# Kernel optimization log

Hardware: AMD Instinct MI355X
Metric: run time of the kernel (lower is better)

Reference implementation:

```python
import jax, jax.numpy as jnp
import numpy as np

EMBED = 1024
HEADS = 16
HEAD_DIM = EMBED // HEADS
SCALE = HEAD_DIM ** -0.5


def setup_inputs() -> dict:
    key = jax.random.key(0)
    ks = jax.random.split(key, 9)
    init = lambda k, shape: jax.random.normal(k, shape, dtype=jnp.float32) * 0.02
    return {
        "hidden_states": jax.random.normal(ks[0], (32, 257, EMBED), dtype=jnp.float32),
        "Wq": init(ks[1], (EMBED, EMBED)), "bq": init(ks[2], (EMBED,)),
        "Wk": init(ks[3], (EMBED, EMBED)), "bk": init(ks[4], (EMBED,)),
        "Wv": init(ks[5], (EMBED, EMBED)), "bv": init(ks[6], (EMBED,)),
        "Wo": init(ks[7], (EMBED, EMBED)), "bo": init(ks[8], (EMBED,)),
    }


def reference(hidden_states, Wq, bq, Wk, bk, Wv, bv, Wo, bo):
    b, t, d = hidden_states.shape
    # projections (torch Linear: x @ W.T + b); scale applied to Q
    q = (hidden_states @ Wq.T + bq) * SCALE
    k = hidden_states @ Wk.T + bk
    v = hidden_states @ Wv.T + bv
    # [b, h, t, hd]
    q = q.reshape(b, t, HEADS, HEAD_DIM).transpose(0, 2, 1, 3)
    k = k.reshape(b, t, HEADS, HEAD_DIM).transpose(0, 2, 1, 3)
    v = v.reshape(b, t, HEADS, HEAD_DIM).transpose(0, 2, 1, 3)
    # attention scores + softmax (dropout p is a no-op in eval mode)
    scores = jnp.einsum("bhqd,bhkd->bhqk", q, k)
    probs = jax.nn.softmax(scores, axis=-1)
    ctx = jnp.einsum("bhqk,bhkd->bhqd", probs, v)
    ctx = ctx.transpose(0, 2, 1, 3).reshape(b, t, d)
    return ctx @ Wo.T + bo
```

## Files before the change

### kernel.cpp

```cpp
#include <hip/hip_runtime.h>


#define B_   32
#define T_   257
#define TP   272
#define H_   16
#define HD_  64
#define D_   1024
#define NTOK 8224
#define BH_  512
#define FRAG_PER_BH 17408

typedef __bf16 bf16;
typedef __bf16 bf16x4 __attribute__((ext_vector_type(4)));
typedef __bf16 bf16x8 __attribute__((ext_vector_type(8)));
typedef short  s16x4  __attribute__((ext_vector_type(4)));
typedef short  s16x8  __attribute__((ext_vector_type(8)));
typedef float  floatx4 __attribute__((ext_vector_type(4)));

static constexpr size_t SZ_XB   = (size_t)NTOK * D_ * 2;
static constexpr size_t SZ_WQKV = (size_t)3 * D_ * D_ * 2;
static constexpr size_t SZ_W    = (size_t)D_ * D_ * 2;
static constexpr size_t SZ_QK   = (size_t)BH_ * FRAG_PER_BH * 2;

static constexpr size_t OFF_XB   = 0;
static constexpr size_t OFF_WQKV = OFF_XB + SZ_XB;
static constexpr size_t OFF_WO   = OFF_WQKV + SZ_WQKV;
static constexpr size_t OFF_Q    = OFF_WO + SZ_W;
static constexpr size_t OFF_K    = OFF_Q + SZ_QK;
static constexpr size_t OFF_V    = OFF_K + SZ_QK;
static constexpr size_t OFF_CTX  = OFF_V + SZ_QK;

#define GLD16(gp, lp)                                                        \
  __builtin_amdgcn_global_load_lds(                                          \
      (const __attribute__((address_space(1))) void*)(gp),                   \
      (__attribute__((address_space(3))) void*)(lp), 16, 0, 0)

__global__ void cast_all_kernel(const float* __restrict__ hs,
                                const float* __restrict__ Wq, const float* __restrict__ Wk,
                                const float* __restrict__ Wv, const float* __restrict__ Wo,
                                bf16* __restrict__ xb, bf16* __restrict__ wqkv,
                                bf16* __restrict__ wob) {
  const int y = blockIdx.y;
  const float* s;
  bf16* d;
  int n4;
  if (y == 0) {
    s = hs; d = xb; n4 = NTOK * D_ / 4;
  } else {
    int z = y - 1;
    s = (z == 0) ? Wq : (z == 1) ? Wk : (z == 2) ? Wv : Wo;
    d = (z < 3) ? wqkv + (size_t)z * D_ * D_ : wob;
    n4 = D_ * D_ / 4;
  }
  int i = blockIdx.x * blockDim.x + threadIdx.x;
  int stride = gridDim.x * blockDim.x;
  for (int idx = i; idx < n4; idx += stride) {
    float4 v = reinterpret_cast<const float4*>(s)[idx];
    bf16x4 o;
    o[0] = (bf16)v.x; o[1] = (bf16)v.y; o[2] = (bf16)v.z; o[3] = (bf16)v.w;
    reinterpret_cast<bf16x4*>(d)[idx] = o;
  }
}



#define KTILE(TT, CC)                                                        \
  do {                                                                       \
    const int ktn_ = ((TT) + 2 < 32) ? (TT) + 2 : 31;                        \
    _Pragma("unroll") for (int mi_ = 0; mi_ < 4; mi_++)                      \
      af[mi_] = *reinterpret_cast<const bf16x8*>(                            \
          smem + (CC) * 8192 + (arow + mi_ * 16) * 32 + qsw);                \
    _Pragma("unroll") for (int nj_ = 0; nj_ < 4; nj_++)                      \
      bfr[nj_] = *reinterpret_cast<const bf16x8*>(                           \
          smem + 16384 + (CC) * 4096 + (brow + nj_ * 16) * 32 + qsw);        \
    asm volatile("s_waitcnt lgkmcnt(0)" ::: "memory");                       \
    __builtin_amdgcn_sched_barrier(0);                                       \
    __builtin_amdgcn_s_barrier();                                            \
                       \
    GLD16(aSrc0 + ktn_ * 32, dstA0 + (CC) * 8192);                           \
    GLD16(aSrc1 + ktn_ * 32, dstA1 + (CC) * 8192);                           \
    GLD16(bSrc + ktn_ * 32, dstB + (CC) * 4096);                             \
    __builtin_amdgcn_sched_barrier(0);                                       \
    __builtin_amdgcn_s_setprio(1);                                           \
    _Pragma("unroll") for (int mi_ = 0; mi_ < 4; mi_++)                      \
      _Pragma("unroll") for (int nj_ = 0; nj_ < 4; nj_++)                    \
        acc[mi_][nj_] = __builtin_amdgcn_mfma_f32_16x16x32_bf16(             \
            af[mi_], bfr[nj_], acc[mi_][nj_], 0, 0, 0);                      \
    __builtin_amdgcn_s_setprio(0);                                           \
    asm volatile("s_waitcnt vmcnt(3)" ::: "memory");                         \
    __builtin_amdgcn_s_barrier();                                            \
  } while (0)

__global__ __launch_bounds__(512, 4) void qkv_gemm(
    const bf16* __restrict__ xb, const bf16* __restrict__ wqkv,
    const float* __restrict__ bq, const float* __restrict__ bk,
    const float* __restrict__ bv,
    bf16* __restrict__ Qf, bf16* __restrict__ Kf, bf16* __restrict__ Vf) {
  __shared__ bf16 smem[24576];

  const int linear = blockIdx.x;
  const int mt = linear / 24, nt = linear % 24;
  const int m0 = mt * 256, n0 = nt * 128;
  const int tid = threadIdx.x;
  const int lane = tid & 63, w = tid >> 6;
  const int n15 = lane & 15, quad = lane >> 4;
  const int wr4 = w >> 1, wn = w & 1;

  const int arow = wr4 * 64 + n15;
  const int brow = wn * 64 + n15;
  const int qsw = (quad ^ ((n15 >> 1) & 3)) * 8;

  const int srow = lane >> 2;
  const int sseg = ((lane & 3) ^ ((lane >> 3) & 3)) * 8;
  int gmA0 = m0 + (w * 2 + 0) * 16 + srow; if (gmA0 > NTOK - 1) gmA0 = NTOK - 1;
  int gmA1 = m0 + (w * 2 + 1) * 16 + srow; if (gmA1 > NTOK - 1) gmA1 = NTOK - 1;
  const bf16* aSrc0 = xb + (size_t)gmA0 * D_ + sseg;
  const bf16* aSrc1 = xb + (size_t)gmA1 * D_ + sseg;
  const bf16* bSrc  = wqkv + (size_t)(n0 + w * 16 + srow) * D_ + sseg;
  bf16* dstA0 = smem + (w * 2 + 0) * 512;
  bf16* dstA1 = smem + (w * 2 + 1) * 512;
  bf16* dstB  = smem + 16384 + w * 512;

  floatx4 acc[4][4] = {};
  bf16x8 af[4], bfr[4];

  GLD16(aSrc0, dstA0); GLD16(aSrc1, dstA1); GLD16(bSrc, dstB);
  GLD16(aSrc0 + 32, dstA0 + 8192); GLD16(aSrc1 + 32, dstA1 + 8192);
  GLD16(bSrc + 32, dstB + 4096);
  asm volatile("s_waitcnt vmcnt(3)" ::: "memory");
  __builtin_amdgcn_s_barrier();

  for (int t = 0; t < 32; t += 2) {
    KTILE(t, 0);
    KTILE(t + 1, 1);
  }

  asm volatile("s_waitcnt vmcnt(0)" ::: "memory");
  __builtin_amdgcn_s_barrier();

  const int z = nt >> 3;
  bf16* zdst = (z == 0) ? Qf : (z == 1) ? Kf : Vf;
  const float scale = (z == 0) ? 0.125f : 1.0f;
  const float* bias = (z == 0) ? bq : (z == 1) ? bk : bv;
  const int znb = (nt & 7) * 128;

  for (int h = 0; h < 2; h++) {
    if ((wr4 >> 1) == h) {
      float bvv[4];
#pragma unroll
      for (int nj = 0; nj < 4; nj++)
        bvv[nj] = bias[znb + wn * 64 + nj * 16 + n15];
#pragma unroll
      for (int mi = 0; mi < 4; mi++)
#pragma unroll
        for (int nj = 0; nj < 4; nj++) {
          int colL = wn * 64 + nj * 16 + n15;
#pragma unroll
          for (int r = 0; r < 4; r++) {
            int rowL = (wr4 & 1) * 64 + mi * 16 + quad * 4 + r;
            smem[rowL * 136 + colL] = (bf16)((acc[mi][nj][r] + bvv[nj]) * scale);
          }
        }
    }
    __syncthreads();

    const int mh0 = m0 + h * 128;
    int nU = 0, nA = 0, tgA0 = 0, tA = 0, tEndA = 0, tEndB = 0, bA = 0;
    int span = NTOK - mh0;
    if (span > 0) {
      if (span > 128) span = 128;
      bA = mh0 / T_;
      tA = mh0 - bA * T_;
      tEndA = (tA + span < T_) ? tA + span : T_;
      tgA0 = tA >> 4;
      nA = ((tEndA - 1) >> 4) - tgA0 + 1;
      nU = nA;
      if (tA + span > T_ && bA + 1 < B_) {
        tEndB = tA + span - T_;
        nU += ((tEndB - 1) >> 4) + 1;
      }
    }

    for (int u = w; u < nU * 2; u += 8) {
      int g = u >> 1, hh = u & 1;
      int bb, tg, tlo, thi;
      if (g < nA) {
        bb = bA; tg = tgA0 + g;
        tlo = (tA > tg * 16) ? tA : tg * 16;
        int te = tg * 16 + 16; thi = (te < tEndA) ? te : tEndA;
      } else {
        bb = bA + 1; tg = g - nA; tlo = tg * 16;
        int te = tg * 16 + 16; thi = (te < tEndB) ? te : tEndB;
      }
      const int hgl = (nt & 7) * 2 + hh;
      bf16* gb = zdst + (size_t)(bb * H_ + hgl) * FRAG_PER_BH + tg * 1024;
      const int hc = hh * 64;
      if (z != 2) {
        int ki = lane & 15, dc = lane >> 4;
        int tt = tg * 16 + ki;
        if (tt >= tlo && tt < thi) {
          int rowL = bb * T_ + tt - mh0;
          bf16x8 v0 = *reinterpret_cast<const bf16x8*>(smem + rowL * 136 + hc + dc * 8);
          bf16x8 v1 = *reinterpret_cast<const bf16x8*>(smem + rowL * 136 + hc + 32 + dc * 8);
          *reinterpret_cast<bf16x8*>(gb + dc * 128 + ki * 8) = v0;
          *reinterpret_cast<bf16x8*>(gb + 512 + dc * 128 + ki * 8) = v1;
        }
      } else {
        int q2 = (lane >> 4) & 3, d16 = lane & 15;
        int tb = tg * 16 + q2 * 4;
        bool full = (tb >= tlo) && (tb + 3 < thi);
#pragma unroll
        for (int p = 0; p < 2; p++) {
          bf16x8 vv;
#pragma unroll
          for (int dp = 0; dp < 2; dp++)
#pragma unroll
            for (int ki = 0; ki < 4; ki++) {
              int tt = tb + ki;
              int rr = (bb * T_ + tt - mh0) & 127;
              vv[dp * 4 + ki] = smem[rr * 136 + hc + p * 32 + dp * 16 + d16];
            }
          bf16* cp = gb + (p * 4 + q2) * 128 + d16 * 8;
          if (full) {
            *reinterpret_cast<bf16x8*>(cp) = vv;
          } else {
#pragma unroll
            for (int dp = 0; dp < 2; dp++)
#pragma unroll
              for (int ki = 0; ki < 4; ki++) {
                int tt = tb + ki;
                if (tt >= tlo && tt < thi) cp[dp * 4 + ki] = vv[dp * 4 + ki];
              }
          }
        }
      }
    }
    __syncthreads();
  }
}

__global__ __launch_bounds__(256) void attn_kernel(
    const bf16* __restrict__ Qf, const bf16* __restrict__ Kf,
    const bf16* __restrict__ Vf, bf16* __restrict__ ctx) {
  __shared__ bf16 smem[34816];

  const int bh = blockIdx.x;
  const int tid = threadIdx.x;
  const int lane = tid & 63, w = tid >> 6;
  const int n15 = lane & 15, quad = lane >> 4;
  const int b = bh >> 4, h = bh & 15;

  const bf16* Qb = Qf + (size_t)bh * FRAG_PER_BH;
  const bf16* Kb = Kf + (size_t)bh * FRAG_PER_BH;
  const bf16* Vb = Vf + (size_t)bh * FRAG_PER_BH;

#pragma unroll
  for (int j = 0; j < 17; j++) {
    int c = w * 17 + j;
    const bf16* src = (c < 34) ? (Kb + c * 512) : (Vb + (c - 34) * 512);
    GLD16(src + lane * 8, smem + c * 512);
  }
  __syncthreads();
  const bf16* Ksh = smem;
  const bf16* Vsh = smem + 17408;

  const int fo = quad * 128 + n15 * 8;

  for (int qt = w; qt < 17; qt += 4) {
    bf16x8 qb0 = *reinterpret_cast<const bf16x8*>(Qb + qt * 1024 + fo);
    bf16x8 qb1 = *reinterpret_cast<const bf16x8*>(Qb + qt * 1024 + 512 + fo);

    floatx4 s[17];
#pragma unroll
    for (int kt = 0; kt < 17; kt++) {
      bf16x8 ka0 = *reinterpret_cast<const bf16x8*>(Ksh + kt * 1024 + fo);
      bf16x8 ka1 = *reinterpret_cast<const bf16x8*>(Ksh + kt * 1024 + 512 + fo);
      floatx4 c = {};
      c = __builtin_amdgcn_mfma_f32_16x16x32_bf16(ka0, qb0, c, 0, 0, 0);
      c = __builtin_amdgcn_mfma_f32_16x16x32_bf16(ka1, qb1, c, 0, 0, 0);
      s[kt] = c;
    }
    s[16][1] = -1e30f; s[16][2] = -1e30f; s[16][3] = -1e30f;
    if (quad != 0) s[16][0] = -1e30f;

    float m0 = -1e30f;
#pragma unroll
    for (int kt = 0; kt < 17; kt++)
#pragma unroll
      for (int r = 0; r < 4; r++) m0 = fmaxf(m0, s[kt][r]);
    m0 = fmaxf(m0, __shfl_xor(m0, 16));
    m0 = fmaxf(m0, __shfl_xor(m0, 32));

    float sum = 0.f;
    s16x4 pb[17];
#pragma unroll
    for (int kt = 0; kt < 17; kt++) {
      bf16x4 ph;
#pragma unroll
      for (int r = 0; r < 4; r++) {
        float p = __expf(s[kt][r] - m0);
        sum += p;
        ph[r] = (bf16)p;
      }
      pb[kt] = __builtin_bit_cast(s16x4, ph);
    }
    sum += __shfl_xor(sum, 16);
    sum += __shfl_xor(sum, 32);

    floatx4 o[4] = {};
#pragma unroll
    for (int kt = 0; kt < 17; kt++) {
#pragma unroll
      for (int p = 0; p < 2; p++) {
        bf16x8 vv = *reinterpret_cast<const bf16x8*>(
            Vsh + ((kt * 2 + p) * 4 + quad) * 128 + n15 * 8);
        s16x8 v16 = __builtin_bit_cast(s16x8, vv);
        s16x4 vlo = __builtin_shufflevector(v16, v16, 0, 1, 2, 3);
        s16x4 vhi = __builtin_shufflevector(v16, v16, 4, 5, 6, 7);
        o[p * 2]     = __builtin_amdgcn_mfma_f32_16x16x16bf16_1k(vlo, pb[kt], o[p * 2], 0, 0, 0);
        o[p * 2 + 1] = __builtin_amdgcn_mfma_f32_16x16x16bf16_1k(vhi, pb[kt], o[p * 2 + 1], 0, 0, 0);
      }
    }

    int q = qt * 16 + n15;
    if (q < T_) {
      float inv = 1.0f / sum;
      size_t ob = ((size_t)(b * T_ + q)) * D_ + h * 64 + quad * 4;
#pragma unroll
      for (int dt = 0; dt < 4; dt++) {
        bf16x4 ov;
#pragma unroll
        for (int r = 0; r < 4; r++) ov[r] = (bf16)(o[dt][r] * inv);
        *reinterpret_cast<bf16x4*>(ctx + ob + dt * 16) = ov;
      }
    }
  }
}

__global__ __launch_bounds__(256) void o_gemm(
    const bf16* __restrict__ ctx, const bf16* __restrict__ wo,
    const float* __restrict__ bo, float* __restrict__ out) {
  __shared__ bf16 Ash[128 * 32];
  __shared__ bf16 Bsh[128 * 32];

  const int linear = blockIdx.x;
  const int nbase = (linear & 7) * 128;
  const int mbase = (linear >> 3) * 128;
  const int tid = threadIdx.x;
  const int lane = tid & 63;
  const int w = tid >> 6;
  const int wr = w >> 1, wc = w & 1;
  const int n15 = lane & 15, quad = lane >> 4;

  const int lrow = lane >> 2;
  const int lseg = ((lane & 3) ^ ((lane >> 3) & 3)) * 8;
  const int qsw = (quad ^ ((n15 >> 1) & 3)) * 8;

  floatx4 acc[4][4] = {};

  for (int k0 = 0; k0 < D_; k0 += 32) {
#pragma unroll
    for (int c = 0; c < 2; c++) {
      int r0 = w * 32 + c * 16;
      int row = r0 + lrow;
      int gm = mbase + row; if (gm > NTOK - 1) gm = NTOK - 1;
      GLD16(ctx + (size_t)gm * D_ + k0 + lseg, Ash + r0 * 32);
      GLD16(wo + (size_t)(nbase + row) * D_ + k0 + lseg, Bsh + r0 * 32);
    }
    __syncthreads();
    bf16x8 af[4], bfr[4];
#pragma unroll
    for (int i = 0; i < 4; i++) {
      af[i]  = *reinterpret_cast<const bf16x8*>(Ash + (wr * 64 + i * 16 + n15) * 32 + qsw);
      bfr[i] = *reinterpret_cast<const bf16x8*>(Bsh + (wc * 64 + i * 16 + n15) * 32 + qsw);
    }
#pragma unroll
    for (int i = 0; i < 4; i++)
#pragma unroll
      for (int j = 0; j < 4; j++)
        acc[i][j] = __builtin_amdgcn_mfma_f32_16x16x32_bf16(af[i], bfr[j], acc[i][j], 0, 0, 0);
    __syncthreads();
  }

#pragma unroll
  for (int i = 0; i < 4; i++) {
    int rowb = mbase + wr * 64 + i * 16 + quad * 4;
#pragma unroll
    for (int j = 0; j < 4; j++) {
      int col = nbase + wc * 64 + j * 16 + n15;
      float bval = bo[col];
#pragma unroll
      for (int r = 0; r < 4; r++) {
        int m = rowb + r;
        if (m < NTOK) out[(size_t)m * D_ + col] = acc[i][j][r] + bval;
      }
    }
  }
}

extern "C" void kernel_launch(void* const* d_in, const int* in_sizes, int n_in,
                              void* d_out, int out_size, void* d_ws, size_t ws_size,
                              hipStream_t stream) {
  const float* hs = (const float*)d_in[0];
  const float* Wq = (const float*)d_in[1];
  const float* bq = (const float*)d_in[2];
  const float* Wk = (const float*)d_in[3];
  const float* bk = (const float*)d_in[4];
  const float* Wv = (const float*)d_in[5];
  const float* bv = (const float*)d_in[6];
  const float* Wo = (const float*)d_in[7];
  const float* bo = (const float*)d_in[8];

  char* ws = (char*)d_ws;
  bf16* xb   = (bf16*)(ws + OFF_XB);
  bf16* wqkv = (bf16*)(ws + OFF_WQKV);
  bf16* wob  = (bf16*)(ws + OFF_WO);
  bf16* Qfw  = (bf16*)(ws + OFF_Q);
  bf16* Kfw  = (bf16*)(ws + OFF_K);
  bf16* Vfw  = (bf16*)(ws + OFF_V);
  bf16* ctx  = (bf16*)(ws + OFF_CTX);

  cast_all_kernel<<<dim3(512, 5), 256, 0, stream>>>(hs, Wq, Wk, Wv, Wo,
                                                    xb, wqkv, wob);

  qkv_gemm<<<792, 512, 0, stream>>>(xb, wqkv, bq, bk, bv, Qfw, Kfw, Vfw);
  attn_kernel<<<BH_, 256, 0, stream>>>(Qfw, Kfw, Vfw, ctx);
  o_gemm<<<520, 256, 0, stream>>>(ctx, wob, bo, (float*)d_out);
}
```

Baseline: 234.8 us.

## Split attention per query tile, drop LDS staging, and double-buffer the output GEMM

The attention kernel now gives each wavefront its own (batch-head, query-tile) pair across 2176 blocks, with an XCD-aware block swizzle. K and V are read straight from global memory instead of being staged in shared memory, which raises parallelism but repeats K/V reads across the 17 query tiles. The QKV epilogue now writes zeros into padded V rows so the unstaged reads stay correct. The output GEMM uses a two-stage shared-memory double buffer with prefetch two tiles ahead, explicit waitcnt, barriers and setprio, so loads overlap with MFMA work.

```diff
diff --git a/kernel.cpp b/kernel.cpp
--- a/kernel.cpp
+++ b/kernel.cpp
@@ -231,6 +231,7 @@
               for (int ki = 0; ki < 4; ki++) {
                 int tt = tb + ki;
                 if (tt >= tlo && tt < thi) cp[dp * 4 + ki] = vv[dp * 4 + ki];
+                else if (tt >= T_)         cp[dp * 4 + ki] = (bf16)0.0f;
               }
           }
         }
@@ -243,106 +244,119 @@
 __global__ __launch_bounds__(256) void attn_kernel(
     const bf16* __restrict__ Qf, const bf16* __restrict__ Kf,
     const bf16* __restrict__ Vf, bf16* __restrict__ ctx) {
-  __shared__ bf16 smem[34816];
-
-  const int bh = blockIdx.x;
+  const int bsw = (int)(blockIdx.x & 7) * 272 + (int)(blockIdx.x >> 3);
   const int tid = threadIdx.x;
   const int lane = tid & 63, w = tid >> 6;
+  const int gw = bsw * 4 + w;
+  const int bh = gw / 17, qt = gw - bh * 17;
   const int n15 = lane & 15, quad = lane >> 4;
   const int b = bh >> 4, h = bh & 15;
 
   const bf16* Qb = Qf + (size_t)bh * FRAG_PER_BH;
   const bf16* Kb = Kf + (size_t)bh * FRAG_PER_BH;
   const bf16* Vb = Vf + (size_t)bh * FRAG_PER_BH;
-
-#pragma unroll
-  for (int j = 0; j < 17; j++) {
-    int c = w * 17 + j;
-    const bf16* src = (c < 34) ? (Kb + c * 512) : (Vb + (c - 34) * 512);
-    GLD16(src + lane * 8, smem + c * 512);
-  }
-  __syncthreads();
-  const bf16* Ksh = smem;
-  const bf16* Vsh = smem + 17408;
-
   const int fo = quad * 128 + n15 * 8;
 
-  for (int qt = w; qt < 17; qt += 4) {
-    bf16x8 qb0 = *reinterpret_cast<const bf16x8*>(Qb + qt * 1024 + fo);
-    bf16x8 qb1 = *reinterpret_cast<const bf16x8*>(Qb + qt * 1024 + 512 + fo);
-
-    floatx4 s[17];
-#pragma unroll
-    for (int kt = 0; kt < 17; kt++) {
-      bf16x8 ka0 = *reinterpret_cast<const bf16x8*>(Ksh + kt * 1024 + fo);
-      bf16x8 ka1 = *reinterpret_cast<const bf16x8*>(Ksh + kt * 1024 + 512 + fo);
-      floatx4 c = {};
-      c = __builtin_amdgcn_mfma_f32_16x16x32_bf16(ka0, qb0, c, 0, 0, 0);
-      c = __builtin_amdgcn_mfma_f32_16x16x32_bf16(ka1, qb1, c, 0, 0, 0);
-      s[kt] = c;
-    }
-    s[16][1] = -1e30f; s[16][2] = -1e30f; s[16][3] = -1e30f;
-    if (quad != 0) s[16][0] = -1e30f;
-
-    float m0 = -1e30f;
-#pragma unroll
-    for (int kt = 0; kt < 17; kt++)
-#pragma unroll
-      for (int r = 0; r < 4; r++) m0 = fmaxf(m0, s[kt][r]);
-    m0 = fmaxf(m0, __shfl_xor(m0, 16));
-    m0 = fmaxf(m0, __shfl_xor(m0, 32));
-
-    float sum = 0.f;
-    s16x4 pb[17];
-#pragma unroll
-    for (int kt = 0; kt < 17; kt++) {
-      bf16x4 ph;
-#pragma unroll
-      for (int r = 0; r < 4; r++) {
-        float p = __expf(s[kt][r] - m0);
-        sum += p;
-        ph[r] = (bf16)p;
-      }
-      pb[kt] = __builtin_bit_cast(s16x4, ph);
-    }
-    sum += __shfl_xor(sum, 16);
-    sum += __shfl_xor(sum, 32);
-
-    floatx4 o[4] = {};
-#pragma unroll
-    for (int kt = 0; kt < 17; kt++) {
-#pragma unroll
-      for (int p = 0; p < 2; p++) {
-        bf16x8 vv = *reinterpret_cast<const bf16x8*>(
-            Vsh + ((kt * 2 + p) * 4 + quad) * 128 + n15 * 8);
-        s16x8 v16 = __builtin_bit_cast(s16x8, vv);
-        s16x4 vlo = __builtin_shufflevector(v16, v16, 0, 1, 2, 3);
-        s16x4 vhi = __builtin_shufflevector(v16, v16, 4, 5, 6, 7);
-        o[p * 2]     = __builtin_amdgcn_mfma_f32_16x16x16bf16_1k(vlo, pb[kt], o[p * 2], 0, 0, 0);
-        o[p * 2 + 1] = __builtin_amdgcn_mfma_f32_16x16x16bf16_1k(vhi, pb[kt], o[p * 2 + 1], 0, 0, 0);
-      }
-    }
-
-    int q = qt * 16 + n15;
-    if (q < T_) {
-      float inv = 1.0f / sum;
-      size_t ob = ((size_t)(b * T_ + q)) * D_ + h * 64 + quad * 4;
-#pragma unroll
-      for (int dt = 0; dt < 4; dt++) {
-        bf16x4 ov;
-#pragma unroll
-        for (int r = 0; r < 4; r++) ov[r] = (bf16)(o[dt][r] * inv);
-        *reinterpret_cast<bf16x4*>(ctx + ob + dt * 16) = ov;
-      }
+  bf16x8 qb0 = *reinterpret_cast<const bf16x8*>(Qb + qt * 1024 + fo);
+  bf16x8 qb1 = *reinterpret_cast<const bf16x8*>(Qb + qt * 1024 + 512 + fo);
+
+  floatx4 s[17];
+#pragma unroll
+  for (int kt = 0; kt < 17; kt++) {
+    bf16x8 ka0 = *reinterpret_cast<const bf16x8*>(Kb + kt * 1024 + fo);
+    bf16x8 ka1 = *reinterpret_cast<const bf16x8*>(Kb + kt * 1024 + 512 + fo);
+    floatx4 c = {};
+    c = __builtin_amdgcn_mfma_f32_16x16x32_bf16(ka0, qb0, c, 0, 0, 0);
+    c = __builtin_amdgcn_mfma_f32_16x16x32_bf16(ka1, qb1, c, 0, 0, 0);
+    s[kt] = c;
+  }
+  s[16][1] = -1e30f; s[16][2] = -1e30f; s[16][3] = -1e30f;
+  if (quad != 0) s[16][0] = -1e30f;
+
+  float m0 = -1e30f;
+#pragma unroll
+  for (int kt = 0; kt < 17; kt++)
+#pragma unroll
+    for (int r = 0; r < 4; r++) m0 = fmaxf(m0, s[kt][r]);
+  m0 = fmaxf(m0, __shfl_xor(m0, 16));
+  m0 = fmaxf(m0, __shfl_xor(m0, 32));
+
+  float sum = 0.f;
+  s16x4 pb[17];
+#pragma unroll
+  for (int kt = 0; kt < 17; kt++) {
+    bf16x4 ph;
+#pragma unroll
+    for (int r = 0; r < 4; r++) {
+      float p = __expf(s[kt][r] - m0);
+      sum += p;
+      ph[r] = (bf16)p;
+    }
+    pb[kt] = __builtin_bit_cast(s16x4, ph);
+  }
+  sum += __shfl_xor(sum, 16);
+  sum += __shfl_xor(sum, 32);
+
+  floatx4 o[4] = {};
+#pragma unroll
+  for (int kt = 0; kt < 17; kt++) {
+#pragma unroll
+    for (int p = 0; p < 2; p++) {
+      bf16x8 vv = *reinterpret_cast<const bf16x8*>(
+          Vb + ((kt * 2 + p) * 4 + quad) * 128 + n15 * 8);
+      s16x8 v16 = __builtin_bit_cast(s16x8, vv);
+      s16x4 vlo = __builtin_shufflevector(v16, v16, 0, 1, 2, 3);
+      s16x4 vhi = __builtin_shufflevector(v16, v16, 4, 5, 6, 7);
+      o[p * 2]     = __builtin_amdgcn_mfma_f32_16x16x16bf16_1k(vlo, pb[kt], o[p * 2], 0, 0, 0);
+      o[p * 2 + 1] = __builtin_amdgcn_mfma_f32_16x16x16bf16_1k(vhi, pb[kt], o[p * 2 + 1], 0, 0, 0);
+    }
+  }
+
+  int q = qt * 16 + n15;
+  if (q < T_) {
+    float inv = 1.0f / sum;
+    size_t ob = ((size_t)(b * T_ + q)) * D_ + h * 64 + quad * 4;
+#pragma unroll
+    for (int dt = 0; dt < 4; dt++) {
+      bf16x4 ov;
+#pragma unroll
+      for (int r = 0; r < 4; r++) ov[r] = (bf16)(o[dt][r] * inv);
+      *reinterpret_cast<bf16x4*>(ctx + ob + dt * 16) = ov;
     }
   }
 }
+
+#define KTILE_O(TT, CC)                                                      \
+  do {                                                                       \
+    const int ktn_ = ((TT) + 2 < 32) ? (TT) + 2 : 31;                        \
+    _Pragma("unroll") for (int i_ = 0; i_ < 4; i_++) {                       \
+      af[i_]  = *reinterpret_cast<const bf16x8*>(                            \
+          smem + (CC) * 4096 + (wr * 64 + i_ * 16 + n15) * 32 + qsw);        \
+      bfr[i_] = *reinterpret_cast<const bf16x8*>(                            \
+          smem + 8192 + (CC) * 4096 + (wc * 64 + i_ * 16 + n15) * 32 + qsw); \
+    }                                                                        \
+    asm volatile("s_waitcnt lgkmcnt(0)" ::: "memory");                       \
+    __builtin_amdgcn_sched_barrier(0);                                       \
+    __builtin_amdgcn_s_barrier();                                            \
+    GLD16(aS0 + ktn_ * 32, dA0 + (CC) * 4096);                               \
+    GLD16(aS1 + ktn_ * 32, dA1 + (CC) * 4096);                               \
+    GLD16(bS0 + ktn_ * 32, dB0 + (CC) * 4096);                               \
+    GLD16(bS1 + ktn_ * 32, dB1 + (CC) * 4096);                               \
+    __builtin_amdgcn_sched_barrier(0);                                       \
+    __builtin_amdgcn_s_setprio(1);                                           \
+    _Pragma("unroll") for (int i_ = 0; i_ < 4; i_++)                         \
+      _Pragma("unroll") for (int j_ = 0; j_ < 4; j_++)                       \
+        acc[i_][j_] = __builtin_amdgcn_mfma_f32_16x16x32_bf16(               \
+            af[i_], bfr[j_], acc[i_][j_], 0, 0, 0);                          \
+    __builtin_amdgcn_s_setprio(0);                                           \
+    asm volatile("s_waitcnt vmcnt(4)" ::: "memory");                         \
+    __builtin_amdgcn_s_barrier();                                            \
+  } while (0)
 
 __global__ __launch_bounds__(256) void o_gemm(
     const bf16* __restrict__ ctx, const bf16* __restrict__ wo,
     const float* __restrict__ bo, float* __restrict__ out) {
-  __shared__ bf16 Ash[128 * 32];
-  __shared__ bf16 Bsh[128 * 32];
+  __shared__ bf16 smem[16384];
 
   const int linear = blockIdx.x;
   const int nbase = (linear & 7) * 128;
@@ -357,31 +371,31 @@
   const int lseg = ((lane & 3) ^ ((lane >> 3) & 3)) * 8;
   const int qsw = (quad ^ ((n15 >> 1) & 3)) * 8;
 
+  int gm0 = mbase + w * 32 + lrow;      if (gm0 > NTOK - 1) gm0 = NTOK - 1;
+  int gm1 = mbase + w * 32 + 16 + lrow; if (gm1 > NTOK - 1) gm1 = NTOK - 1;
+  const bf16* aS0 = ctx + (size_t)gm0 * D_ + lseg;
+  const bf16* aS1 = ctx + (size_t)gm1 * D_ + lseg;
+  const bf16* bS0 = wo + (size_t)(nbase + w * 32 + lrow) * D_ + lseg;
+  const bf16* bS1 = wo + (size_t)(nbase + w * 32 + 16 + lrow) * D_ + lseg;
+  bf16* dA0 = smem + (w * 32) * 32;
+  bf16* dA1 = smem + (w * 32 + 16) * 32;
+  bf16* dB0 = smem + 8192 + (w * 32) * 32;
+  bf16* dB1 = smem + 8192 + (w * 32 + 16) * 32;
+
   floatx4 acc[4][4] = {};
-
-  for (int k0 = 0; k0 < D_; k0 += 32) {
-#pragma unroll
-    for (int c = 0; c < 2; c++) {
-      int r0 = w * 32 + c * 16;
-      int row = r0 + lrow;
-      int gm = mbase + row; if (gm > NTOK - 1) gm = NTOK - 1;
-      GLD16(ctx + (size_t)gm * D_ + k0 + lseg, Ash + r0 * 32);
-      GLD16(wo + (size_t)(nbase + row) * D_ + k0 + lseg, Bsh + r0 * 32);
-    }
-    __syncthreads();
-    bf16x8 af[4], bfr[4];
-#pragma unroll
-    for (int i = 0; i < 4; i++) {
-      af[i]  = *reinterpret_cast<const bf16x8*>(Ash + (wr * 64 + i * 16 + n15) * 32 + qsw);
-      bfr[i] = *reinterpret_cast<const bf16x8*>(Bsh + (wc * 64 + i * 16 + n15) * 32 + qsw);
-    }
-#pragma unroll
-    for (int i = 0; i < 4; i++)
-#pragma unroll
-      for (int j = 0; j < 4; j++)
-        acc[i][j] = __builtin_amdgcn_mfma_f32_16x16x32_bf16(af[i], bfr[j], acc[i][j], 0, 0, 0);
-    __syncthreads();
-  }
+  bf16x8 af[4], bfr[4];
+
+  GLD16(aS0, dA0); GLD16(aS1, dA1); GLD16(bS0, dB0); GLD16(bS1, dB1);
+  GLD16(aS0 + 32, dA0 + 4096); GLD16(aS1 + 32, dA1 + 4096);
+  GLD16(bS0 + 32, dB0 + 4096); GLD16(bS1 + 32, dB1 + 4096);
+  asm volatile("s_waitcnt vmcnt(4)" ::: "memory");
+  __builtin_amdgcn_s_barrier();
+
+  for (int t = 0; t < 32; t += 2) {
+    KTILE_O(t, 0);
+    KTILE_O(t + 1, 1);
+  }
+  asm volatile("s_waitcnt vmcnt(0)" ::: "memory");
 
 #pragma unroll
   for (int i = 0; i < 4; i++) {
@@ -425,6 +439,6 @@
                                                     xb, wqkv, wob);
 
   qkv_gemm<<<792, 512, 0, stream>>>(xb, wqkv, bq, bk, bv, Qfw, Kfw, Vfw);
-  attn_kernel<<<BH_, 256, 0, stream>>>(Qfw, Kfw, Vfw, ctx);
+  attn_kernel<<<2176, 256, 0, stream>>>(Qfw, Kfw, Vfw, ctx);
   o_gemm<<<520, 256, 0, stream>>>(ctx, wob, bo, (float*)d_out);
 }
```

After: 258.3 us. +10.0%, slower.
